# Performance work log

Hardware: AMD Instinct MI355X
Metric: run time of the kernel (lower is better)

## Reference

```python
import jax, jax.numpy as jnp
import numpy as np

B, H, I, E = 16, 16, 512, 512  # batch, heads, input_dim, embedding_dim (I must == E for matmul(q,k))


def setup_inputs() -> dict:
    key = jax.random.key(0)
    k_x, k_q, k_k, k_v, k_w, k_b = jax.random.split(key, 6)
    return {
        "x": jax.random.normal(k_x, (B, 1, I, E), dtype=jnp.float32),
        "W_q": jax.random.normal(k_q, (1, H, I, E), dtype=jnp.float32),
        "W_k": jax.random.normal(k_k, (1, H, I, E), dtype=jnp.float32),
        "W_v": jax.random.normal(k_v, (1, H, I, E), dtype=jnp.float32),
        "mlp_w": jax.random.normal(k_w, (E, E), dtype=jnp.float32) * (1.0 / np.sqrt(E)),
        "mlp_b": jnp.zeros((E,), dtype=jnp.float32),
    }


def reference(x, W_q, W_k, W_v, mlp_w, mlp_b):
    # Broadcast elementwise "projections": [B,1,I,E] * [1,H,I,E] -> [B,H,I,E]
    q = x * W_q
    k = x * W_k
    v = x * W_v
    scale = jnp.sqrt(jnp.asarray(E, dtype=x.dtype))
    # matmul with NO transpose of keys (as in the original): [B,H,I,E]@[B,H,I,E] needs E==I
    scores = jnp.matmul(q, k) / scale            # [B,H,I,I]
    attn = jax.nn.softmax(scores, axis=2)        # softmax over dim=2 (rows), faithful to source
    emb = jnp.sum(jnp.matmul(attn, v), axis=2)   # [B,H,I,E] summed over I -> [B,H,E]
    return emb @ mlp_w.T + mlp_b                 # nn.Linear: x @ W^T + b -> [B,H,E]
```

## Files before the change

kernel.cpp:

```cpp
#include <hip/hip_runtime.h>

#define B_ 16
#define H_ 16
#define I_ 512
#define E_ 512


#define NSLICE 16
#define KSPLIT 8

__global__ __launch_bounds__(256) void k_emb_part(const float* __restrict__ x,
                                                  const float* __restrict__ Wv,
                                                  float* __restrict__ part) {
    const int e     = blockIdx.x * 64 + (threadIdx.x & 63);
    const int b0    = blockIdx.y * 8;
    const int h0    = (blockIdx.z & 1) * 8;
    const int slice = blockIdx.z >> 1;
    const int lane  = threadIdx.x & 63;
    const int wave  = threadIdx.x >> 6;

    float acc[8][8];
#pragma unroll
    for (int bi = 0; bi < 8; ++bi)
#pragma unroll
        for (int hj = 0; hj < 8; ++hj) acc[bi][hj] = 0.0f;

    const int ibase = slice * 32 + wave * 8;
    const float* xp[8];
    const float* wp[8];
#pragma unroll
    for (int bi = 0; bi < 8; ++bi)
        xp[bi] = x + ((size_t)(b0 + bi) * I_ + ibase) * E_ + e;
#pragma unroll
    for (int hj = 0; hj < 8; ++hj)
        wp[hj] = Wv + ((size_t)(h0 + hj) * I_ + ibase) * E_ + e;

    for (int ii = 0; ii < 8; ++ii) {
        const int off = ii * E_;
        float xv[8], wv[8];
#pragma unroll
        for (int bi = 0; bi < 8; ++bi) xv[bi] = xp[bi][off];
#pragma unroll
        for (int hj = 0; hj < 8; ++hj) wv[hj] = wp[hj][off];
#pragma unroll
        for (int bi = 0; bi < 8; ++bi)
#pragma unroll
            for (int hj = 0; hj < 8; ++hj)
                acc[bi][hj] = fmaf(xv[bi], wv[hj], acc[bi][hj]);
    }

    __shared__ float red[4][64][64];
#pragma unroll
    for (int bi = 0; bi < 8; ++bi)
#pragma unroll
        for (int hj = 0; hj < 8; ++hj)
            red[wave][bi * 8 + hj][lane] = acc[bi][hj];
    __syncthreads();

    for (int t = threadIdx.x; t < 64 * 64; t += 256) {
        const int pair = t >> 6, le = t & 63;
        float s = (red[0][pair][le] + red[1][pair][le]) +
                  (red[2][pair][le] + red[3][pair][le]);
        const int row = (b0 + (pair >> 3)) * H_ + h0 + (pair & 7);
        part[((size_t)slice * (B_ * H_) + row) * E_ + blockIdx.x * 64 + le] = s;
    }
}

__global__ __launch_bounds__(256) void k_emb_reduce(const float4* __restrict__ part,
                                                    float4* __restrict__ emb) {
    const int idx = blockIdx.x * 256 + threadIdx.x;
    const int sl  = (B_ * H_ * E_) / 4;
    float4 s = part[idx];
#pragma unroll
    for (int j = 1; j < NSLICE; ++j) {
        float4 p = part[(size_t)j * sl + idx];
        s.x += p.x; s.y += p.y; s.z += p.z; s.w += p.w;
    }
    emb[idx] = s;
}

__global__ __launch_bounds__(256) void k_mlp_part(const float* __restrict__ emb,
                                                  const float* __restrict__ W,
                                                  float* __restrict__ part) {
    const int cblk = blockIdx.x;
    const int rblk = blockIdx.y;
    const int kch  = blockIdx.z;
    const int k0   = kch * 64;

    __shared__ float As[64][68];
    __shared__ float Ws[64][68];

    const int t = threadIdx.x;

#pragma unroll
    for (int it = 0; it < 4; ++it) {
        const int f = t + it * 256;
        const int r = f >> 4, kq = f & 15;
        float4 v = *(const float4*)(emb + (size_t)(rblk * 64 + r) * E_ + k0 + kq * 4);
        *(float4*)&As[r][((kq ^ (r >> 2)) & 15) * 4] = v;
    }
#pragma unroll
    for (int it = 0; it < 4; ++it) {
        const int f = t + it * 256;
        const int c = f >> 4, kq = f & 15;
        float4 v = *(const float4*)(W + (size_t)(cblk * 64 + c) * E_ + k0 + kq * 4);
        const int pc = (((c >> 2) ^ kq) & 15) * 4 + (c & 3);
        Ws[kq * 4 + 0][pc] = v.x;
        Ws[kq * 4 + 1][pc] = v.y;
        Ws[kq * 4 + 2][pc] = v.z;
        Ws[kq * 4 + 3][pc] = v.w;
    }
    __syncthreads();

    const int tx = t & 15, ty = t >> 4;
    const int c0 = tx * 4, r0 = ty * 4;

    float4 acc0 = {0, 0, 0, 0}, acc1 = {0, 0, 0, 0};
    float4 acc2 = {0, 0, 0, 0}, acc3 = {0, 0, 0, 0};

    for (int k = 0; k < 64; k += 4) {
        const int K  = k >> 2;
        const int ac = ((K ^ ty) & 15) * 4;
        const int wc = ((tx ^ K) & 15) * 4;
        float4 a0 = *(const float4*)&As[r0 + 0][ac];
        float4 a1 = *(const float4*)&As[r0 + 1][ac];
        float4 a2 = *(const float4*)&As[r0 + 2][ac];
        float4 a3 = *(const float4*)&As[r0 + 3][ac];
        float4 w0 = *(const float4*)&Ws[k + 0][wc];
        float4 w1 = *(const float4*)&Ws[k + 1][wc];
        float4 w2 = *(const float4*)&Ws[k + 2][wc];
        float4 w3 = *(const float4*)&Ws[k + 3][wc];
#define MLP_STEP(ACC, AV)                                                  \
        ACC.x = fmaf(AV.x, w0.x, fmaf(AV.y, w1.x, fmaf(AV.z, w2.x, fmaf(AV.w, w3.x, ACC.x)))); \
        ACC.y = fmaf(AV.x, w0.y, fmaf(AV.y, w1.y, fmaf(AV.z, w2.y, fmaf(AV.w, w3.y, ACC.y)))); \
        ACC.z = fmaf(AV.x, w0.z, fmaf(AV.y, w1.z, fmaf(AV.z, w2.z, fmaf(AV.w, w3.z, ACC.z)))); \
        ACC.w = fmaf(AV.x, w0.w, fmaf(AV.y, w1.w, fmaf(AV.z, w2.w, fmaf(AV.w, w3.w, ACC.w))));
        MLP_STEP(acc0, a0)
        MLP_STEP(acc1, a1)
        MLP_STEP(acc2, a2)
        MLP_STEP(acc3, a3)
#undef MLP_STEP
    }

    float* dst = part + ((size_t)kch * (B_ * H_) + rblk * 64 + r0) * E_ +
                 cblk * 64 + c0;
    *(float4*)(dst + 0 * E_) = acc0;
    *(float4*)(dst + 1 * E_) = acc1;
    *(float4*)(dst + 2 * E_) = acc2;
    *(float4*)(dst + 3 * E_) = acc3;
}

__global__ __launch_bounds__(256) void k_out(const float4* __restrict__ part,
                                             const float4* __restrict__ bias,
                                             float4* __restrict__ out) {
    const int idx = blockIdx.x * 256 + threadIdx.x;
    const int sl  = (B_ * H_ * E_) / 4;
    float4 s = part[idx];
#pragma unroll
    for (int j = 1; j < KSPLIT; ++j) {
        float4 p = part[(size_t)j * sl + idx];
        s.x += p.x; s.y += p.y; s.z += p.z; s.w += p.w;
    }
    float4 bv = bias[idx & (E_ / 4 - 1)];
    s.x += bv.x; s.y += bv.y; s.z += bv.z; s.w += bv.w;
    out[idx] = s;
}

extern "C" void kernel_launch(void* const* d_in, const int* in_sizes, int n_in,
                              void* d_out, int out_size, void* d_ws, size_t ws_size,
                              hipStream_t stream) {
    const float* x     = (const float*)d_in[0];
    const float* W_v   = (const float*)d_in[3];
    const float* mlp_w = (const float*)d_in[4];
    const float* mlp_b = (const float*)d_in[5];
    float* out = (float*)d_out;

    float* epart = (float*)d_ws;
    float* emb   = epart + (size_t)NSLICE * B_ * H_ * E_;
    float* mpart = emb + (size_t)B_ * H_ * E_;

    dim3 g1(E_ / 64, B_ / 8, (H_ / 8) * NSLICE);
    k_emb_part<<<g1, 256, 0, stream>>>(x, W_v, epart);

    k_emb_reduce<<<(B_ * H_ * E_ / 4) / 256, 256, 0, stream>>>(
        (const float4*)epart, (float4*)emb);

    dim3 g3(E_ / 64, (B_ * H_) / 64, KSPLIT);
    k_mlp_part<<<g3, 256, 0, stream>>>(emb, mlp_w, mpart);

    k_out<<<(B_ * H_ * E_ / 4) / 256, 256, 0, stream>>>(
        (const float4*)mpart, (const float4*)mlp_b, (float4*)out);
}
```

Before: 111.9 us.

## Stage x and W_v tiles in shared memory and split b/h across waves

The emb partial kernel is reorganised so each block covers all 16 batches and all 16 heads for one e-tile and one i-slice. The x and W_v rows are staged through LDS with float4 loads, and each wave computes a different 8x8 (b,h) sub-tile instead of a different i-range. Each global element is now loaded once per block rather than by every (b,h) block, and the cross-wave LDS reduction goes away. In exchange the grid shrinks to 128 blocks, which lowers parallelism, and the loop adds chunked __syncthreads barriers plus 64 KB of shared memory per block.

Result: slower. 116.2 us (+3.8%).

```diff
diff --git a/kernel.cpp b/kernel.cpp
--- a/kernel.cpp
+++ b/kernel.cpp
@@ -12,12 +12,17 @@
 __global__ __launch_bounds__(256) void k_emb_part(const float* __restrict__ x,
                                                   const float* __restrict__ Wv,
                                                   float* __restrict__ part) {
-    const int e     = blockIdx.x * 64 + (threadIdx.x & 63);
-    const int b0    = blockIdx.y * 8;
-    const int h0    = (blockIdx.z & 1) * 8;
-    const int slice = blockIdx.z >> 1;
-    const int lane  = threadIdx.x & 63;
-    const int wave  = threadIdx.x >> 6;
+    const int etile = blockIdx.x;
+    const int slice = blockIdx.y;
+    const int t     = (int)threadIdx.x;
+    const int lane  = t & 63;
+    const int wave  = t >> 6;
+    const int e     = etile * 64 + lane;
+    const int b0    = (wave & 1) * 8;
+    const int h0    = (wave >> 1) * 8;
+
+    __shared__ float xs[8][16][64];
+    __shared__ float ws[8][16][64];
 
     float acc[8][8];
 #pragma unroll
@@ -25,45 +30,47 @@
 #pragma unroll
         for (int hj = 0; hj < 8; ++hj) acc[bi][hj] = 0.0f;
 
-    const int ibase = slice * 32 + wave * 8;
-    const float* xp[8];
-    const float* wp[8];
+    const int ibase0 = slice * 32;
+
+    for (int chunk = 0; chunk < 4; ++chunk) {
+        const int ib = ibase0 + chunk * 8;
+        if (chunk) __syncthreads();
+#pragma unroll
+        for (int it2 = 0; it2 < 8; ++it2) {
+            const int f  = t + it2 * 256;
+            const int ii = f >> 8;
+            const int bb = (f >> 4) & 15;
+            const int eq = f & 15;
+            const size_t goff = ((size_t)bb * I_ + (ib + ii)) * E_ + etile * 64 + eq * 4;
+            float4 vx = *(const float4*)(x + goff);
+            float4 vw = *(const float4*)(Wv + goff);
+            *(float4*)&xs[ii][bb][eq * 4] = vx;
+            *(float4*)&ws[ii][bb][eq * 4] = vw;
+        }
+        __syncthreads();
+
+#pragma unroll
+        for (int ii = 0; ii < 8; ++ii) {
+            float xv[8], wv[8];
+#pragma unroll
+            for (int bi = 0; bi < 8; ++bi) xv[bi] = xs[ii][b0 + bi][lane];
+#pragma unroll
+            for (int hj = 0; hj < 8; ++hj) wv[hj] = ws[ii][h0 + hj][lane];
+#pragma unroll
+            for (int bi = 0; bi < 8; ++bi)
+#pragma unroll
+                for (int hj = 0; hj < 8; ++hj)
+                    acc[bi][hj] = fmaf(xv[bi], wv[hj], acc[bi][hj]);
+        }
+    }
+
 #pragma unroll
     for (int bi = 0; bi < 8; ++bi)
-        xp[bi] = x + ((size_t)(b0 + bi) * I_ + ibase) * E_ + e;
-#pragma unroll
-    for (int hj = 0; hj < 8; ++hj)
-        wp[hj] = Wv + ((size_t)(h0 + hj) * I_ + ibase) * E_ + e;
-
-    for (int ii = 0; ii < 8; ++ii) {
-        const int off = ii * E_;
-        float xv[8], wv[8];
-#pragma unroll
-        for (int bi = 0; bi < 8; ++bi) xv[bi] = xp[bi][off];
-#pragma unroll
-        for (int hj = 0; hj < 8; ++hj) wv[hj] = wp[hj][off];
-#pragma unroll
-        for (int bi = 0; bi < 8; ++bi)
-#pragma unroll
-            for (int hj = 0; hj < 8; ++hj)
-                acc[bi][hj] = fmaf(xv[bi], wv[hj], acc[bi][hj]);
-    }
-
-    __shared__ float red[4][64][64];
-#pragma unroll
-    for (int bi = 0; bi < 8; ++bi)
-#pragma unroll
-        for (int hj = 0; hj < 8; ++hj)
-            red[wave][bi * 8 + hj][lane] = acc[bi][hj];
-    __syncthreads();
-
-    for (int t = threadIdx.x; t < 64 * 64; t += 256) {
-        const int pair = t >> 6, le = t & 63;
-        float s = (red[0][pair][le] + red[1][pair][le]) +
-                  (red[2][pair][le] + red[3][pair][le]);
-        const int row = (b0 + (pair >> 3)) * H_ + h0 + (pair & 7);
-        part[((size_t)slice * (B_ * H_) + row) * E_ + blockIdx.x * 64 + le] = s;
-    }
+#pragma unroll
+        for (int hj = 0; hj < 8; ++hj) {
+            const int row = (b0 + bi) * H_ + h0 + hj;
+            part[((size_t)slice * (B_ * H_) + row) * E_ + e] = acc[bi][hj];
+        }
 }
 
 __global__ __launch_bounds__(256) void k_emb_reduce(const float4* __restrict__ part,
@@ -179,7 +186,7 @@
     float* emb   = epart + (size_t)NSLICE * B_ * H_ * E_;
     float* mpart = emb + (size_t)B_ * H_ * E_;
 
-    dim3 g1(E_ / 64, B_ / 8, (H_ / 8) * NSLICE);
+    dim3 g1(E_ / 64, NSLICE);
     k_emb_part<<<g1, 256, 0, stream>>>(x, W_v, epart);
 
     k_emb_reduce<<<(B_ * H_ * E_ / 4) / 256, 256, 0, stream>>>(
```
